# Kernel optimization log

Measured on AMD Instinct MI355X. Metric: run time of the kernel, lower is better.

The kernel has to match this reference:

```python
import jax, jax.numpy as jnp
import numpy as np

B, H, W, C = 64, 56, 56, 256
ROUTES = 4
CONV_OUT = 64


def setup_inputs() -> dict:
    key = jax.random.key(0)
    k1, k2, k3 = jax.random.split(key, 3)
    inputs = jax.random.normal(k1, (B, H, W, C), dtype=jnp.float32)
    # he_normal init for conv kernel (HWIO), zeros bias (keras defaults)
    fan_in = 3 * 3 * C
    conv_w = jax.random.normal(k2, (3, 3, C, CONV_OUT), dtype=jnp.float32) * np.sqrt(2.0 / fan_in)
    conv_b = jnp.zeros((CONV_OUT,), dtype=jnp.float32)
    # glorot_uniform for dense (keras default)
    limit = np.sqrt(6.0 / (CONV_OUT + ROUTES))
    fc_w = jax.random.uniform(k3, (CONV_OUT, ROUTES), dtype=jnp.float32, minval=-limit, maxval=limit)
    fc_b = jnp.zeros((ROUTES,), dtype=jnp.float32)
    return {"inputs": inputs, "conv_w": conv_w, "conv_b": conv_b, "fc_w": fc_w, "fc_b": fc_b}


def reference(inputs, conv_w, conv_b, fc_w, fc_b):
    routes = fc_b.shape[0]
    # route predictor: conv 3x3 stride 2 valid -> global avg pool -> dense logits
    y = jax.lax.conv_general_dilated(
        inputs, conv_w, window_strides=(2, 2), padding="VALID",
        dimension_numbers=("NHWC", "HWIO", "NHWC"))
    y = y + conv_b  # (B, H', W', 64)
    pooled = jnp.mean(y, axis=(1, 2))  # (B, 64)
    logits = pooled @ fc_w + fc_b      # (B, routes)
    route_width = inputs.shape[-1] // routes
    route = jnp.argmax(logits, axis=-1)  # (B,)
    # per-example channel-group gather: channels [r*w, (r+1)*w)
    idx = route[:, None] * route_width + jnp.arange(route_width)  # (B, w)
    x = jnp.take_along_axis(inputs, idx[:, None, None, :], axis=-1)  # (B, H, W, w)
    return (x, logits)
```

## Files before the change

### kernel.cpp

```cpp
#include <hip/hip_runtime.h>
#include <cstdint>
#include <cstddef>

#define Bn 64
#define Hn 56
#define Wn 56
#define Cn 256
#define COn 64
#define RWn 64
#define XSZ ((size_t)Bn * Hn * Wn * RWn)

__device__ __forceinline__ void f4add(float4& a, const float4& v) {
    a.x += v.x; a.y += v.y; a.z += v.z; a.w += v.w;
}
__device__ __forceinline__ float4 f4sub(const float4& a, const float4& b) {
    return make_float4(a.x - b.x, a.y - b.y, a.z - b.z, a.w - b.w);
}
__device__ __forceinline__ void f4fma(float4& a, float s, const float4& v) {
    a.x += s * v.x; a.y += s * v.y; a.z += s * v.z; a.w += s * v.w;
}

__global__ __launch_bounds__(256) void kA_bins(
        const float* __restrict__ in, float* __restrict__ spart,
        int NS, int RPS) {
    const int blk   = blockIdx.x;
    const int b     = blk / NS;
    const int split = blk - b * NS;
    const int tid   = threadIdx.x;
    const int lane  = tid & 63;
    const int wave  = tid >> 6;

    const float* base = in + (size_t)b * (Hn * Wn * Cn) + (size_t)lane * 4
                           + (size_t)wave * Cn;

    float4 acc[9];
#pragma unroll
    for (int k = 0; k < 9; ++k) acc[k] = make_float4(0.f, 0.f, 0.f, 0.f);

    const int h0 = split * RPS;
    for (int h = h0; h < h0 + RPS; ++h) {
        const bool  he  = (h & 1) == 0;
        const float rh0 = (he  && h <= 52)           ? 1.f : 0.f;
        const float rh1 = (!he && h <= 53)           ? 1.f : 0.f;
        const float rh2 = (he  && h >= 2 && h <= 54) ? 1.f : 0.f;
        if (rh0 == 0.f && rh1 == 0.f && rh2 == 0.f) continue;

        const float* rowp = base + (size_t)h * (Wn * Cn);
        float4 R  = make_float4(0.f, 0.f, 0.f, 0.f);
        float4 e0 = R, e1 = R;
#pragma unroll
        for (int wb = 0; wb < Wn; wb += 4) {
            if (wb == 52 && wave == 3) continue;
            const float4 v = *(const float4*)(rowp + (size_t)wb * Cn);
            if (wb == 0)  e0 = v;
            if (wb == 52) e1 = v;
            f4add(R, v);
        }

        const float rhE[3] = { rh0, rh1, rh2 };
        if ((wave & 1) == 0) {
            float4 cA, cB;
            if (wave == 0) { cA = R;            cB = f4sub(R, e0); }
            else           { cA = f4sub(R, e1); cB = R;            }
#pragma unroll
            for (int kh = 0; kh < 3; ++kh) {
                f4fma(acc[kh * 3 + 0], rhE[kh], cA);
                f4fma(acc[kh * 3 + 2], rhE[kh], cB);
            }
        } else {
#pragma unroll
            for (int kh = 0; kh < 3; ++kh)
                f4fma(acc[kh * 3 + 1], rhE[kh], R);
        }
    }

    __shared__ float4 lds4[4][9][64];
#pragma unroll
    for (int k = 0; k < 9; ++k) lds4[wave][k][lane] = acc[k];
    __syncthreads();

    const float* ldsf = (const float*)lds4;
    float* op = spart + (((size_t)b * NS + split) * 9) * 256;
#pragma unroll
    for (int k = 0; k < 9; ++k) {
        const float s = ldsf[(0 * 9 + k) * 256 + tid] + ldsf[(1 * 9 + k) * 256 + tid]
                      + ldsf[(2 * 9 + k) * 256 + tid] + ldsf[(3 * 9 + k) * 256 + tid];
        op[k * 256 + tid] = s;
    }
}

__global__ __launch_bounds__(256) void kB_logits(
        const float* __restrict__ spart,
        const float* __restrict__ convw, const float* __restrict__ convb,
        const float* __restrict__ fcw,   const float* __restrict__ fcb,
        float* __restrict__ out_logits, int* __restrict__ routes, int NS) {
    const int b = blockIdx.x;
    const int t = threadIdx.x;
    __shared__ float sS[9 * 256];
    __shared__ float pP[4][64];
    __shared__ float pld[64];
    __shared__ float lgt[4];

#pragma unroll
    for (int k = 0; k < 9; ++k) {
        float a = 0.f;
#pragma unroll 7
        for (int s = 0; s < NS; ++s)
            a += spart[(((size_t)b * NS + s) * 9 + k) * 256 + t];
        sS[k * 256 + t] = a;
    }
    __syncthreads();

    {
        const int co = t & 63, part = t >> 6;
        float a = 0.f;
#pragma unroll
        for (int k = 0; k < 9; ++k) {
            const int cb = part * 64;
#pragma unroll 8
            for (int ci = 0; ci < 64; ++ci)
                a += sS[k * 256 + cb + ci] * convw[(size_t)(k * 256 + cb + ci) * 64 + co];
        }
        pP[part][co] = a;
    }
    __syncthreads();

    if (t < 64) {
        pld[t] = (pP[0][t] + pP[1][t] + pP[2][t] + pP[3][t]) * (1.f / 729.f) + convb[t];
    }
    __syncthreads();

    if (t < 4) {
        float a = fcb[t];
#pragma unroll
        for (int co = 0; co < 64; ++co) a += pld[co] * fcw[co * 4 + t];
        lgt[t] = a;
        out_logits[b * 4 + t] = a;
    }
    __syncthreads();

    if (t == 0) {
        int bi = 0; float best = lgt[0];
#pragma unroll
        for (int r = 1; r < 4; ++r) if (lgt[r] > best) { best = lgt[r]; bi = r; }
        routes[b] = bi;
    }
}

__global__ __launch_bounds__(256) void kC_gather(
        const float* __restrict__ in, const int* __restrict__ routes,
        float* __restrict__ out) {
    const size_t idx = (size_t)blockIdx.x * 256 + threadIdx.x;
    const size_t pix = idx >> 4;
    const int   f4i  = (int)(idx & 15);
    const int   b    = (int)(pix / (Hn * Wn));
    const int   r    = routes[b];
    const float4 v = *(const float4*)(in + pix * (size_t)Cn + (size_t)r * RWn + (size_t)f4i * 4);
    ((float4*)out)[idx] = v;
}

extern "C" void kernel_launch(void* const* d_in, const int* in_sizes, int n_in,
                              void* d_out, int out_size, void* d_ws, size_t ws_size,
                              hipStream_t stream) {
    const float* in    = (const float*)d_in[0];
    const float* convw = (const float*)d_in[1];
    const float* convb = (const float*)d_in[2];
    const float* fcw   = (const float*)d_in[3];
    const float* fcb   = (const float*)d_in[4];
    float* out = (float*)d_out;

    int NS = 1;
    const int cand[5] = {14, 8, 4, 2, 1};
    for (int i = 0; i < 5; ++i) {
        const size_t need = (size_t)Bn * cand[i] * 9 * 256 * sizeof(float) + 256;
        if (ws_size >= need) { NS = cand[i]; break; }
    }
    const int RPS = Hn / NS;

    float* spart = (float*)d_ws;
    int* routes  = (int*)((char*)d_ws + (size_t)Bn * NS * 9 * 256 * sizeof(float));

    kA_bins  <<<Bn * NS, 256, 0, stream>>>(in, spart, NS, RPS);
    kB_logits<<<Bn,      256, 0, stream>>>(spart, convw, convb, fcw, fcb,
                                           out + XSZ, routes, NS);
    kC_gather<<<12544,   256, 0, stream>>>(in, routes, out);
}
```

Before: 361.4 us.

## Fuse logits reduction into bins kernel via last-block atomic, batch gather work

Merges the logits kernel into the bin-accumulation kernel. Each block bumps a per-batch arrival counter, and the last block to arrive for a batch sums the partials and computes the logits and route. This removes one kernel launch and its dependency gap, at the cost of an extra memset and a fixed split count that no longer checks workspace size. The gather kernel now processes four float4s per thread with a quarter of the blocks.

```diff
diff --git a/kernel.cpp b/kernel.cpp
--- a/kernel.cpp
+++ b/kernel.cpp
@@ -9,6 +9,8 @@
 #define COn 64
 #define RWn 64
 #define XSZ ((size_t)Bn * Hn * Wn * RWn)
+#define NSd 14
+#define RPSd (Hn / NSd)
 
 __device__ __forceinline__ void f4add(float4& a, const float4& v) {
     a.x += v.x; a.y += v.y; a.z += v.z; a.w += v.w;
@@ -20,15 +22,25 @@
     a.x += s * v.x; a.y += s * v.y; a.z += s * v.z; a.w += s * v.w;
 }
 
-__global__ __launch_bounds__(256) void kA_bins(
+__global__ __launch_bounds__(256) void kA_fused(
         const float* __restrict__ in, float* __restrict__ spart,
-        int NS, int RPS) {
+        int* __restrict__ arrival, int* __restrict__ routes,
+        const float* __restrict__ convw, const float* __restrict__ convb,
+        const float* __restrict__ fcw,   const float* __restrict__ fcb,
+        float* __restrict__ out_logits) {
     const int blk   = blockIdx.x;
-    const int b     = blk / NS;
-    const int split = blk - b * NS;
+    const int b     = blk / NSd;
+    const int split = blk - b * NSd;
     const int tid   = threadIdx.x;
     const int lane  = tid & 63;
     const int wave  = tid >> 6;
+
+    __shared__ union SM {
+        float4 lds4[4][9][64];
+        struct { float sS[9 * 256]; float pP[4][64];
+                 float pld[64]; float lgt[4]; } kb;
+    } sm;
+    __shared__ int s_old;
 
     const float* base = in + (size_t)b * (Hn * Wn * Cn) + (size_t)lane * 4
                            + (size_t)wave * Cn;
@@ -37,8 +49,8 @@
 #pragma unroll
     for (int k = 0; k < 9; ++k) acc[k] = make_float4(0.f, 0.f, 0.f, 0.f);
 
-    const int h0 = split * RPS;
-    for (int h = h0; h < h0 + RPS; ++h) {
+    const int h0 = split * RPSd;
+    for (int h = h0; h < h0 + RPSd; ++h) {
         const bool  he  = (h & 1) == 0;
         const float rh0 = (he  && h <= 52)           ? 1.f : 0.f;
         const float rh1 = (!he && h <= 53)           ? 1.f : 0.f;
@@ -74,40 +86,37 @@
         }
     }
 
-    __shared__ float4 lds4[4][9][64];
 #pragma unroll
-    for (int k = 0; k < 9; ++k) lds4[wave][k][lane] = acc[k];
+    for (int k = 0; k < 9; ++k) sm.lds4[wave][k][lane] = acc[k];
     __syncthreads();
 
-    const float* ldsf = (const float*)lds4;
-    float* op = spart + (((size_t)b * NS + split) * 9) * 256;
+    {
+        const float* ldsf = (const float*)sm.lds4;
+        float* op = spart + (((size_t)b * NSd + split) * 9) * 256;
 #pragma unroll
-    for (int k = 0; k < 9; ++k) {
-        const float s = ldsf[(0 * 9 + k) * 256 + tid] + ldsf[(1 * 9 + k) * 256 + tid]
-                      + ldsf[(2 * 9 + k) * 256 + tid] + ldsf[(3 * 9 + k) * 256 + tid];
-        op[k * 256 + tid] = s;
+        for (int k = 0; k < 9; ++k) {
+            const float s = ldsf[(0 * 9 + k) * 256 + tid] + ldsf[(1 * 9 + k) * 256 + tid]
+                          + ldsf[(2 * 9 + k) * 256 + tid] + ldsf[(3 * 9 + k) * 256 + tid];
+            op[k * 256 + tid] = s;
+        }
     }
-}
+    __syncthreads();
 
-__global__ __launch_bounds__(256) void kB_logits(
-        const float* __restrict__ spart,
-        const float* __restrict__ convw, const float* __restrict__ convb,
-        const float* __restrict__ fcw,   const float* __restrict__ fcb,
-        float* __restrict__ out_logits, int* __restrict__ routes, int NS) {
-    const int b = blockIdx.x;
-    const int t = threadIdx.x;
-    __shared__ float sS[9 * 256];
-    __shared__ float pP[4][64];
-    __shared__ float pld[64];
-    __shared__ float lgt[4];
+    if (tid == 0) {
+        s_old = __hip_atomic_fetch_add(&arrival[b], 1,
+                                       __ATOMIC_ACQ_REL, __HIP_MEMORY_SCOPE_AGENT);
+    }
+    __syncthreads();
+    if (s_old != NSd - 1) return;
 
+    const int t = tid;
 #pragma unroll
     for (int k = 0; k < 9; ++k) {
         float a = 0.f;
-#pragma unroll 7
-        for (int s = 0; s < NS; ++s)
-            a += spart[(((size_t)b * NS + s) * 9 + k) * 256 + t];
-        sS[k * 256 + t] = a;
+#pragma unroll
+        for (int s = 0; s < NSd; ++s)
+            a += spart[(((size_t)b * NSd + s) * 9 + k) * 256 + t];
+        sm.kb.sS[k * 256 + t] = a;
     }
     __syncthreads();
 
@@ -119,30 +128,30 @@
             const int cb = part * 64;
 #pragma unroll 8
             for (int ci = 0; ci < 64; ++ci)
-                a += sS[k * 256 + cb + ci] * convw[(size_t)(k * 256 + cb + ci) * 64 + co];
+                a += sm.kb.sS[k * 256 + cb + ci] * convw[(size_t)(k * 256 + cb + ci) * 64 + co];
         }
-        pP[part][co] = a;
+        sm.kb.pP[part][co] = a;
     }
     __syncthreads();
 
-    if (t < 64) {
-        pld[t] = (pP[0][t] + pP[1][t] + pP[2][t] + pP[3][t]) * (1.f / 729.f) + convb[t];
-    }
+    if (t < 64)
+        sm.kb.pld[t] = (sm.kb.pP[0][t] + sm.kb.pP[1][t] + sm.kb.pP[2][t] + sm.kb.pP[3][t])
+                       * (1.f / 729.f) + convb[t];
     __syncthreads();
 
     if (t < 4) {
         float a = fcb[t];
 #pragma unroll
-        for (int co = 0; co < 64; ++co) a += pld[co] * fcw[co * 4 + t];
-        lgt[t] = a;
+        for (int co = 0; co < 64; ++co) a += sm.kb.pld[co] * fcw[co * 4 + t];
+        sm.kb.lgt[t] = a;
         out_logits[b * 4 + t] = a;
     }
     __syncthreads();
 
     if (t == 0) {
-        int bi = 0; float best = lgt[0];
+        int bi = 0; float best = sm.kb.lgt[0];
 #pragma unroll
-        for (int r = 1; r < 4; ++r) if (lgt[r] > best) { best = lgt[r]; bi = r; }
+        for (int r = 1; r < 4; ++r) if (sm.kb.lgt[r] > best) { best = sm.kb.lgt[r]; bi = r; }
         routes[b] = bi;
     }
 }
@@ -150,13 +159,17 @@
 __global__ __launch_bounds__(256) void kC_gather(
         const float* __restrict__ in, const int* __restrict__ routes,
         float* __restrict__ out) {
-    const size_t idx = (size_t)blockIdx.x * 256 + threadIdx.x;
-    const size_t pix = idx >> 4;
-    const int   f4i  = (int)(idx & 15);
-    const int   b    = (int)(pix / (Hn * Wn));
-    const int   r    = routes[b];
-    const float4 v = *(const float4*)(in + pix * (size_t)Cn + (size_t)r * RWn + (size_t)f4i * 4);
-    ((float4*)out)[idx] = v;
+#pragma unroll
+    for (int k = 0; k < 4; ++k) {
+        const size_t idx = (size_t)blockIdx.x * 1024 + k * 256 + threadIdx.x;
+        const size_t pix = idx >> 4;
+        const int   f4i  = (int)(idx & 15);
+        const int   b    = (int)(pix / (Hn * Wn));
+        const int   r    = routes[b];
+        const float4 v = *(const float4*)(in + pix * (size_t)Cn
+                                          + (size_t)r * RWn + (size_t)f4i * 4);
+        ((float4*)out)[idx] = v;
+    }
 }
 
 extern "C" void kernel_launch(void* const* d_in, const int* in_sizes, int n_in,
@@ -169,19 +182,14 @@
     const float* fcb   = (const float*)d_in[4];
     float* out = (float*)d_out;
 
-    int NS = 1;
-    const int cand[5] = {14, 8, 4, 2, 1};
-    for (int i = 0; i < 5; ++i) {
-        const size_t need = (size_t)Bn * cand[i] * 9 * 256 * sizeof(float) + 256;
-        if (ws_size >= need) { NS = cand[i]; break; }
-    }
-    const int RPS = Hn / NS;
+    const size_t spartBytes = (size_t)Bn * NSd * 9 * 256 * sizeof(float);
+    float* spart   = (float*)d_ws;
+    int*   arrival = (int*)((char*)d_ws + spartBytes);
+    int*   routes  = arrival + Bn;
 
-    float* spart = (float*)d_ws;
-    int* routes  = (int*)((char*)d_ws + (size_t)Bn * NS * 9 * 256 * sizeof(float));
+    hipMemsetAsync(arrival, 0, Bn * sizeof(int), stream);
 
-    kA_bins  <<<Bn * NS, 256, 0, stream>>>(in, spart, NS, RPS);
-    kB_logits<<<Bn,      256, 0, stream>>>(spart, convw, convb, fcw, fcb,
-                                           out + XSZ, routes, NS);
-    kC_gather<<<12544,   256, 0, stream>>>(in, routes, out);
+    kA_fused <<<Bn * NSd, 256, 0, stream>>>(in, spart, arrival, routes,
+                                            convw, convb, fcw, fcb, out + XSZ);
+    kC_gather<<<3136,     256, 0, stream>>>(in, routes, out);
 }
```

Measured after the change: 383.5 us. +6.1%, slower.

## Split row-bin reduction into 28 two-row blocks and unroll gather 4x

Applied to the files above, without the earlier changes.

Adds a specialized reduction kernel where each block handles exactly two input rows (one even, one odd) across 28 splits per batch. Tap masks are applied at store time instead of per-row FMAs, giving 1792 blocks instead of 896 for more parallelism during the full-input read. The gather kernel now has each thread copy four float4s, with a quarter of the blocks. Costs are more partial sums in workspace, which makes the logits kernel's reduction longer, plus a fallback path when the workspace is too small.

```diff
diff --git a/kernel.cpp b/kernel.cpp
--- a/kernel.cpp
+++ b/kernel.cpp
@@ -9,6 +9,7 @@
 #define COn 64
 #define RWn 64
 #define XSZ ((size_t)Bn * Hn * Wn * RWn)
+#define NS2 28
 
 __device__ __forceinline__ void f4add(float4& a, const float4& v) {
     a.x += v.x; a.y += v.y; a.z += v.z; a.w += v.w;
@@ -16,10 +17,74 @@
 __device__ __forceinline__ float4 f4sub(const float4& a, const float4& b) {
     return make_float4(a.x - b.x, a.y - b.y, a.z - b.z, a.w - b.w);
 }
+
+__global__ __launch_bounds__(256, 4) void kA_w2(
+        const float* __restrict__ in, float* __restrict__ spart) {
+    const int blk   = blockIdx.x;
+    const int b     = blk / NS2;
+    const int split = blk - b * NS2;
+    const int tid   = threadIdx.x;
+    const int lane  = tid & 63;
+    const int wave  = tid >> 6;
+
+    const float* base = in + (size_t)b * (Hn * Wn * Cn) + (size_t)lane * 4
+                           + (size_t)wave * Cn + (size_t)(split * 2) * (Wn * Cn);
+
+    float4 z = make_float4(0.f, 0.f, 0.f, 0.f);
+    float4 sA[2] = { z, z };
+    float4 sB[2] = { z, z };
+
+#pragma unroll
+    for (int r = 0; r < 2; ++r) {
+        if (r == 1 && split == NS2 - 1) continue;
+        const float* rowp = base + (size_t)r * (Wn * Cn);
+        float4 R = z, e0 = z, e1 = z;
+#pragma unroll
+        for (int wb = 0; wb < Wn; wb += 4) {
+            if (wb == 52 && wave == 3) continue;
+            const float4 v = *(const float4*)(rowp + (size_t)wb * Cn);
+            if (wb == 0)  e0 = v;
+            if (wb == 52) e1 = v;
+            f4add(R, v);
+        }
+        if ((wave & 1) == 0) {
+            sA[r] = (wave == 0) ? R : f4sub(R, e1);
+            sB[r] = (wave == 0) ? f4sub(R, e0) : R;
+        } else {
+            sA[r] = R;
+        }
+    }
+
+    __shared__ float4 lds[4][4][64];
+    lds[wave][0][lane] = sA[0];
+    lds[wave][1][lane] = sB[0];
+    lds[wave][2][lane] = sA[1];
+    lds[wave][3][lane] = sB[1];
+    __syncthreads();
+
+    const float* f = (const float*)lds;
+    const int t = tid;
+#define LDSF(w, s) f[((w) * 4 + (s)) * 256 + t]
+    const float evenA = LDSF(0, 0) + LDSF(2, 0);
+    const float evenB = LDSF(0, 1) + LDSF(2, 1);
+    const float evenO = LDSF(1, 0) + LDSF(3, 0);
+    const float oddA  = LDSF(0, 2) + LDSF(2, 2);
+    const float oddB  = LDSF(0, 3) + LDSF(2, 3);
+    const float oddO  = LDSF(1, 2) + LDSF(3, 2);
+#undef LDSF
+    const float m0 = (split <= 26) ? 1.f : 0.f;
+    const float m1 = (split <= 26) ? 1.f : 0.f;
+    const float m2 = (split >= 1)  ? 1.f : 0.f;
+
+    float* op = spart + (((size_t)b * NS2 + split) * 9) * 256 + t;
+    op[0 * 256] = evenA * m0;  op[1 * 256] = evenO * m0;  op[2 * 256] = evenB * m0;
+    op[3 * 256] = oddA  * m1;  op[4 * 256] = oddO  * m1;  op[5 * 256] = oddB  * m1;
+    op[6 * 256] = evenA * m2;  op[7 * 256] = evenO * m2;  op[8 * 256] = evenB * m2;
+}
+
 __device__ __forceinline__ void f4fma(float4& a, float s, const float4& v) {
     a.x += s * v.x; a.y += s * v.y; a.z += s * v.z; a.w += s * v.w;
 }
-
 __global__ __launch_bounds__(256) void kA_bins(
         const float* __restrict__ in, float* __restrict__ spart,
         int NS, int RPS) {
@@ -32,7 +97,6 @@
 
     const float* base = in + (size_t)b * (Hn * Wn * Cn) + (size_t)lane * 4
                            + (size_t)wave * Cn;
-
     float4 acc[9];
 #pragma unroll
     for (int k = 0; k < 9; ++k) acc[k] = make_float4(0.f, 0.f, 0.f, 0.f);
@@ -44,7 +108,6 @@
         const float rh1 = (!he && h <= 53)           ? 1.f : 0.f;
         const float rh2 = (he  && h >= 2 && h <= 54) ? 1.f : 0.f;
         if (rh0 == 0.f && rh1 == 0.f && rh2 == 0.f) continue;
-
         const float* rowp = base + (size_t)h * (Wn * Cn);
         float4 R  = make_float4(0.f, 0.f, 0.f, 0.f);
         float4 e0 = R, e1 = R;
@@ -56,7 +119,6 @@
             if (wb == 52) e1 = v;
             f4add(R, v);
         }
-
         const float rhE[3] = { rh0, rh1, rh2 };
         if ((wave & 1) == 0) {
             float4 cA, cB;
@@ -69,8 +131,7 @@
             }
         } else {
 #pragma unroll
-            for (int kh = 0; kh < 3; ++kh)
-                f4fma(acc[kh * 3 + 1], rhE[kh], R);
+            for (int kh = 0; kh < 3; ++kh) f4fma(acc[kh * 3 + 1], rhE[kh], R);
         }
     }
 
@@ -78,7 +139,6 @@
 #pragma unroll
     for (int k = 0; k < 9; ++k) lds4[wave][k][lane] = acc[k];
     __syncthreads();
-
     const float* ldsf = (const float*)lds4;
     float* op = spart + (((size_t)b * NS + split) * 9) * 256;
 #pragma unroll
@@ -104,7 +164,6 @@
 #pragma unroll
     for (int k = 0; k < 9; ++k) {
         float a = 0.f;
-#pragma unroll 7
         for (int s = 0; s < NS; ++s)
             a += spart[(((size_t)b * NS + s) * 9 + k) * 256 + t];
         sS[k * 256 + t] = a;
@@ -125,9 +184,8 @@
     }
     __syncthreads();
 
-    if (t < 64) {
+    if (t < 64)
         pld[t] = (pP[0][t] + pP[1][t] + pP[2][t] + pP[3][t]) * (1.f / 729.f) + convb[t];
-    }
     __syncthreads();
 
     if (t < 4) {
@@ -150,13 +208,17 @@
 __global__ __launch_bounds__(256) void kC_gather(
         const float* __restrict__ in, const int* __restrict__ routes,
         float* __restrict__ out) {
-    const size_t idx = (size_t)blockIdx.x * 256 + threadIdx.x;
-    const size_t pix = idx >> 4;
-    const int   f4i  = (int)(idx & 15);
-    const int   b    = (int)(pix / (Hn * Wn));
-    const int   r    = routes[b];
-    const float4 v = *(const float4*)(in + pix * (size_t)Cn + (size_t)r * RWn + (size_t)f4i * 4);
-    ((float4*)out)[idx] = v;
+#pragma unroll
+    for (int k = 0; k < 4; ++k) {
+        const size_t idx = (size_t)blockIdx.x * 1024 + k * 256 + threadIdx.x;
+        const size_t pix = idx >> 4;
+        const int   f4i  = (int)(idx & 15);
+        const int   b    = (int)(pix / (Hn * Wn));
+        const int   r    = routes[b];
+        const float4 v = *(const float4*)(in + pix * (size_t)Cn
+                                          + (size_t)r * RWn + (size_t)f4i * 4);
+        ((float4*)out)[idx] = v;
+    }
 }
 
 extern "C" void kernel_launch(void* const* d_in, const int* in_sizes, int n_in,
@@ -169,19 +231,27 @@
     const float* fcb   = (const float*)d_in[4];
     float* out = (float*)d_out;
 
-    int NS = 1;
-    const int cand[5] = {14, 8, 4, 2, 1};
-    for (int i = 0; i < 5; ++i) {
-        const size_t need = (size_t)Bn * cand[i] * 9 * 256 * sizeof(float) + 256;
-        if (ws_size >= need) { NS = cand[i]; break; }
-    }
-    const int RPS = Hn / NS;
-
+    const size_t need28 = (size_t)Bn * NS2 * 9 * 256 * sizeof(float) + 256;
     float* spart = (float*)d_ws;
-    int* routes  = (int*)((char*)d_ws + (size_t)Bn * NS * 9 * 256 * sizeof(float));
-
-    kA_bins  <<<Bn * NS, 256, 0, stream>>>(in, spart, NS, RPS);
-    kB_logits<<<Bn,      256, 0, stream>>>(spart, convw, convb, fcw, fcb,
-                                           out + XSZ, routes, NS);
-    kC_gather<<<12544,   256, 0, stream>>>(in, routes, out);
-}
+
+    if (ws_size >= need28) {
+        int* routes = (int*)((char*)d_ws + (size_t)Bn * NS2 * 9 * 256 * sizeof(float));
+        kA_w2    <<<Bn * NS2, 256, 0, stream>>>(in, spart);
+        kB_logits<<<Bn,       256, 0, stream>>>(spart, convw, convb, fcw, fcb,
+                                                out + XSZ, routes, NS2);
+        kC_gather<<<3136,     256, 0, stream>>>(in, routes, out);
+    } else {
+        int NS = 1;
+        const int cand[5] = {14, 8, 4, 2, 1};
+        for (int i = 0; i < 5; ++i) {
+            const size_t need = (size_t)Bn * cand[i] * 9 * 256 * sizeof(float) + 256;
+            if (ws_size >= need) { NS = cand[i]; break; }
+        }
+        const int RPS = Hn / NS;
+        int* routes = (int*)((char*)d_ws + (size_t)Bn * NS * 9 * 256 * sizeof(float));
+        kA_bins  <<<Bn * NS, 256, 0, stream>>>(in, spart, NS, RPS);
+        kB_logits<<<Bn,      256, 0, stream>>>(spart, convw, convb, fcw, fcb,
+                                               out + XSZ, routes, NS);
+        kC_gather<<<3136,    256, 0, stream>>>(in, routes, out);
+    }
+}
```

Result: slower. 400.6 us (+10.8%).
